# Kernel optimization log

Hardware: AMD Instinct MI355X
Metric: run time of the kernel (lower is better)

Reference implementation:

```python
import jax, jax.numpy as jnp
import numpy as np

E = 256
NH = 8
HD = E // NH
N, L, H, W = 8, 300, 96, 96


def setup_inputs() -> dict:
    key = jax.random.key(0)
    ks = jax.random.split(key, 9)
    s = 0.02
    return {
        "query_row": jax.random.normal(ks[0], (N, L, E), jnp.float32),
        "query_col": jax.random.normal(ks[1], (N, L, E), jnp.float32),
        "key_row": jax.random.normal(ks[2], (N, H, W, E), jnp.float32),
        "key_col": jax.random.normal(ks[3], (N, H, W, E), jnp.float32),
        "value": jax.random.normal(ks[4], (N, H, W, E), jnp.float32),
        "in_proj_weight": jax.random.normal(ks[5], (5 * E, E), jnp.float32) * s,
        "in_proj_bias": jax.random.normal(ks[6], (5 * E,), jnp.float32) * s,
        "out_proj_weight": jax.random.normal(ks[7], (E, E), jnp.float32) * s,
        "out_proj_bias": jax.random.normal(ks[8], (E,), jnp.float32) * s,
    }


def reference(query_row, query_col, key_row, key_col, value,
              in_proj_weight, in_proj_bias, out_proj_weight, out_proj_bias):
    n, l, e = query_row.shape
    _, h, w, _ = value.shape
    scale = float(HD) ** -0.5

    def proj(x, i):
        wi = in_proj_weight[i * E:(i + 1) * E]
        bi = in_proj_bias[i * E:(i + 1) * E]
        return x @ wi.T + bi

    q_row = proj(query_row, 0) * scale              # (N,L,E)
    q_col = proj(query_col, 1) * scale              # (N,L,E)
    k_row = proj(key_row, 2).mean(axis=1)           # (N,W,E)  mean over H
    k_col = proj(key_col, 3).mean(axis=2)           # (N,H,E)  mean over W
    v = proj(value, 4)                              # (N,H,W,E)

    qr = q_row.reshape(n, l, NH, HD)
    qc = q_col.reshape(n, l, NH, HD)
    kr = k_row.reshape(n, w, NH, HD)
    kc = k_col.reshape(n, h, NH, HD)
    vh = v.reshape(n, h, w, NH, HD)

    # row/col attention scores, softmax over source axis
    a_row = jax.nn.softmax(jnp.einsum('nled,nwed->nelw', qr, kr), axis=-1)  # (N,NH,L,W)
    a_col = jax.nn.softmax(jnp.einsum('nled,nhed->nelh', qc, kc), axis=-1)  # (N,NH,L,H)

    # col-then-row contraction (original else-branch: src_len_col >= src_len_row)
    out_col = jnp.einsum('nelh,nhwed->nelwd', a_col, vh)   # (N,NH,L,W,HD)
    out = jnp.einsum('nelw,nelwd->nled', a_row, out_col)    # (N,L,NH,HD)

    attn_output = out.transpose(1, 0, 2, 3).reshape(l, n, e)  # (L,N,E)
    return attn_output @ out_proj_weight.T + out_proj_bias
```

## Files before the change

### kernel.cpp

```cpp
#include <hip/hip_runtime.h>
#include <stdint.h>

typedef unsigned short u16;
typedef unsigned int   u32;
typedef __attribute__((ext_vector_type(8))) short bf16x8;
typedef __attribute__((ext_vector_type(4))) float f32x4;

static constexpr float kScale = 0.17677669529663687f;

__device__ __forceinline__ float bfl(u32 dw){ union{u32 u; float f;} x; x.u = dw << 16;        return x.f; }
__device__ __forceinline__ float bfh(u32 dw){ union{u32 u; float f;} x; x.u = dw & 0xffff0000u; return x.f; }
__device__ __forceinline__ float bf2f(u16 v){ union{u32 u; float f;} x; x.u = ((u32)v) << 16;  return x.f; }
__device__ __forceinline__ u16  f2bf(float f){
  union{float f; u32 u;} x; x.f = f;
  u32 r = x.u + 0x7fffu + ((x.u >> 16) & 1u);
  return (u16)(r >> 16);
}

__global__ void detect_kernel(const u16* __restrict__ bias, int* __restrict__ flag){
  int tid = threadIdx.x;
  u16 raw = bias[tid * 2];
  int big = (fabsf(bf2f(raw)) > 1e6f) ? 1 : 0;
  if ((raw & 0x7F80u) == 0x7F80u) big = 1;
  #pragma unroll
  for (int m = 1; m < 64; m <<= 1) big |= __shfl_xor(big, m);
  if (tid == 0) *flag = big;
}

__global__ __launch_bounds__(256) void prep_weights_kernel(
    const void* __restrict__ in_w, const void* __restrict__ out_w,
    u16* __restrict__ Wbf, const int* __restrict__ flag){
  const bool isf32 = (*flag != 0);
  int idx = blockIdx.x * 256 + threadIdx.x;
  size_t off = (size_t)idx * 8;
  const size_t IN_ELEMS = (size_t)1280 * 256;
  bool isout = off >= IN_ELEMS;
  const void* src = isout ? out_w : in_w;
  size_t soff = isout ? off - IN_ELEMS : off;
  u16 xl[8];
  if (isf32){
    const float* p = (const float*)src + soff;
    float4 f0 = *(const float4*)p;
    float4 f1 = *(const float4*)(p + 4);
    xl[0]=f2bf(f0.x); xl[1]=f2bf(f0.y); xl[2]=f2bf(f0.z); xl[3]=f2bf(f0.w);
    xl[4]=f2bf(f1.x); xl[5]=f2bf(f1.y); xl[6]=f2bf(f1.z); xl[7]=f2bf(f1.w);
  } else {
    *(uint4*)xl = *(const uint4*)((const u16*)src + soff);
  }
  *(uint4*)(Wbf + off) = *(uint4*)xl;
}

__global__ void means_kernel(const void* __restrict__ key_row, const void* __restrict__ key_col,
                             float* __restrict__ krm, float* __restrict__ kcm,
                             const int* __restrict__ flag){
  const bool isf32 = (*flag != 0);
  int g   = blockIdx.x * 256 + threadIdx.x;
  int c8  = (g & 31) * 8;
  int ri  = g >> 5;
  int rw  = ri % 96;
  int n   = ri / 96;
  float acc[8];
  #pragma unroll
  for (int i = 0; i < 8; i++) acc[i] = 0.f;

  size_t base, stride;
  const void* src;
  float* dst;
  if (blockIdx.y == 0){
    src    = key_row;
    base   = ((size_t)(n*96)*96 + rw)*256 + c8;
    stride = (size_t)96*256;
    dst    = krm + ((size_t)(n*96) + rw)*256 + c8;
  } else {
    src    = key_col;
    base   = ((size_t)(n*96) + rw)*(size_t)(96*256) + c8;
    stride = 256;
    dst    = kcm + ((size_t)(n*96) + rw)*256 + c8;
  }

  if (isf32){
    const float* p = (const float*)src + base;
    for (int t = 0; t < 96; t++){
      float4 f0 = *(const float4*)(p + t*stride);
      float4 f1 = *(const float4*)(p + t*stride + 4);
      acc[0]+=f0.x; acc[1]+=f0.y; acc[2]+=f0.z; acc[3]+=f0.w;
      acc[4]+=f1.x; acc[5]+=f1.y; acc[6]+=f1.z; acc[7]+=f1.w;
    }
  } else {
    const u16* p = (const u16*)src + base;
    for (int t = 0; t < 96; t++){
      uint4 u = *(const uint4*)(p + t*stride);
      acc[0]+=bfl(u.x); acc[1]+=bfh(u.x); acc[2]+=bfl(u.y); acc[3]+=bfh(u.y);
      acc[4]+=bfl(u.z); acc[5]+=bfh(u.z); acc[6]+=bfl(u.w); acc[7]+=bfh(u.w);
    }
  }
  #pragma unroll
  for (int i = 0; i < 8; i++) dst[i] = acc[i] * (1.f/96.f);
}

template<int XF, int OBF, int OMAP>
__global__ __launch_bounds__(256) void mfma_proj3(
    const void* __restrict__ Xv0, const void* __restrict__ Xv1,
    const u16* __restrict__ Wbf, int wr00, int wr01,
    const void* __restrict__ Bv, int bo0, int bo1,
    void* __restrict__ Yv0, void* __restrict__ Yv1,
    int M, float scale, int head0, int hg,
    const int* __restrict__ flag){
  const bool isf32 = (*flag != 0);
  const bool xf32  = (XF == 0) || (XF == 2 && isf32);
  __shared__ __align__(16) u16 Xs[64*40];
  __shared__ __align__(16) u16 Ws[64*40];
  __shared__ __align__(16) u16 stile[(OMAP==3) ? 64*66 : 64];

  const void* Xv  = blockIdx.z ? Xv1 : Xv0;
  const int wrow0 = blockIdx.z ? wr01 : wr00;
  const int boff  = blockIdx.z ? bo1  : bo0;
  void* Yv        = blockIdx.z ? Yv1 : Yv0;

  int tid = threadIdx.x;
  int m0  = blockIdx.x * 64;
  int j0  = blockIdx.y * 64;
  int wv  = tid >> 6;
  int ln  = tid & 63;
  int l15 = ln & 15;
  int quad = ln >> 4;
  int mh  = wv & 1;
  int nh  = wv >> 1;

  int srow = tid >> 2;
  int sko  = (tid & 3) * 8;

  f32x4 acc[2][2] = {{{0.f,0.f,0.f,0.f},{0.f,0.f,0.f,0.f}},
                     {{0.f,0.f,0.f,0.f},{0.f,0.f,0.f,0.f}}};

  int gm = m0 + srow;
  int wrel = j0 + srow;
  if (OMAP == 3){ wrel += head0*32; if (wrel > 255) wrel = 255; }
  const u16* wsrc = Wbf + (size_t)(wrow0 + wrel)*256 + sko;

  for (int p = 0; p < 8; p++){
    int k0 = p * 32;
    u16 xl[8];
    if (gm < M){
      size_t xoff = (size_t)gm*256 + k0 + sko;
      if (xf32){
        const float* xp = (const float*)Xv + xoff;
        float4 f0 = *(const float4*)xp;
        float4 f1 = *(const float4*)(xp + 4);
        xl[0]=f2bf(f0.x); xl[1]=f2bf(f0.y); xl[2]=f2bf(f0.z); xl[3]=f2bf(f0.w);
        xl[4]=f2bf(f1.x); xl[5]=f2bf(f1.y); xl[6]=f2bf(f1.z); xl[7]=f2bf(f1.w);
      } else {
        *(uint4*)xl = *(const uint4*)((const u16*)Xv + xoff);
      }
    } else {
      #pragma unroll
      for (int i = 0; i < 8; i++) xl[i] = 0;
    }
    uint4 wl = *(const uint4*)(wsrc + k0);
    __syncthreads();
    *(uint4*)(Xs + srow*40 + sko) = *(uint4*)xl;
    *(uint4*)(Ws + srow*40 + sko) = wl;
    __syncthreads();

    bf16x8 a0 = *(const bf16x8*)(Xs + (mh*32 +      l15)*40 + quad*8);
    bf16x8 a1 = *(const bf16x8*)(Xs + (mh*32 + 16 + l15)*40 + quad*8);
    bf16x8 b0 = *(const bf16x8*)(Ws + (nh*32 +      l15)*40 + quad*8);
    bf16x8 b1 = *(const bf16x8*)(Ws + (nh*32 + 16 + l15)*40 + quad*8);
    acc[0][0] = __builtin_amdgcn_mfma_f32_16x16x32_bf16(a0, b0, acc[0][0], 0,0,0);
    acc[0][1] = __builtin_amdgcn_mfma_f32_16x16x32_bf16(a0, b1, acc[0][1], 0,0,0);
    acc[1][0] = __builtin_amdgcn_mfma_f32_16x16x32_bf16(a1, b0, acc[1][0], 0,0,0);
    acc[1][1] = __builtin_amdgcn_mfma_f32_16x16x32_bf16(a1, b1, acc[1][1], 0,0,0);
  }

  float bv[2];
  #pragma unroll
  for (int tj = 0; tj < 2; tj++){
    int bidx = j0 + nh*32 + tj*16 + l15;
    if (OMAP == 3 && bidx > hg*32 - 1) bidx = hg*32 - 1;
    bv[tj] = isf32 ? ((const float*)Bv)[boff + bidx] : bf2f(((const u16*)Bv)[boff + bidx]);
  }

  if (OMAP == 3){
    __syncthreads();
    #pragma unroll
    for (int ti = 0; ti < 2; ti++)
      #pragma unroll
      for (int tj = 0; tj < 2; tj++)
        #pragma unroll
        for (int reg = 0; reg < 4; reg++)
          stile[(mh*32 + ti*16 + quad*4 + reg)*66 + nh*32 + tj*16 + l15] =
              f2bf(scale * (acc[ti][tj][reg] + bv[tj]));
    __syncthreads();
    int hw_i = tid & 63;
    int m    = m0 + hw_i;
    int nn   = m / 9216;
    int hwin = m - nn*9216;
    int hh   = hwin / 96, ww = hwin - hh*96;
    #pragma unroll
    for (int e = 0; e < 16; e++){
      int d_col = (tid >> 6) * 16 + e;
      int col   = j0 + d_col;
      if (col < hg*32){
        int gsv = nn*hg + (col >> 5), d = col & 31;
        ((u16*)Yv)[ (((size_t)gsv*96 + hh)*32 + d)*96 + ww ] = stile[hw_i*66 + d_col];
      }
    }
    return;
  }

  #pragma unroll
  for (int ti = 0; ti < 2; ti++)
    #pragma unroll
    for (int tj = 0; tj < 2; tj++)
      #pragma unroll
      for (int reg = 0; reg < 4; reg++){
        int m = m0 + mh*32 + ti*16 + quad*4 + reg;
        if (m >= M) continue;
        int col = j0 + nh*32 + tj*16 + l15;
        float vval = scale * (acc[ti][tj][reg] + bv[tj]);
        int orow = (OMAP == 1) ? ((m % 300)*8 + (m / 300)) : m;
        size_t oidx = (size_t)orow*256 + col;
        if (OBF == 2){
          if (isf32) ((float*)Yv)[oidx] = vval; else ((u16*)Yv)[oidx] = f2bf(vval);
        } else if (OBF == 1) ((u16*)Yv)[oidx] = f2bf(vval);
        else                 ((float*)Yv)[oidx] = vval;
      }
}

__global__ __launch_bounds__(64) void attn_weights_kernel(
    const u16* __restrict__ qr, const float* __restrict__ kr,
    const u16* __restrict__ qc, const float* __restrict__ kc,
    u16* __restrict__ arow, u16* __restrict__ acol,
    int head0, int hg){
  __shared__ float qs[30*32];
  int lt = blockIdx.x;
  int gs = blockIdx.y;
  int n  = gs / hg;
  int head = head0 + (gs % hg);
  const u16*   q = blockIdx.z ? qc : qr;
  const float* k = blockIdx.z ? kc : kr;
  u16*         a = blockIdx.z ? acol : arow;
  int lane = threadIdx.x;
  int l0   = lt * 30;

  for (int i = lane; i < 960; i += 64){
    int li = i >> 5, d = i & 31;
    qs[i] = bf2f(q[((size_t)(n*300) + l0 + li)*256 + head*32 + d]);
  }

  bool has2 = (lane < 32);
  float k1[32], k2[32];
  {
    const float* kp = k + ((size_t)(n*96) + lane)*256 + head*32;
    #pragma unroll
    for (int d4 = 0; d4 < 8; d4++){
      float4 f = *(const float4*)(kp + d4*4);
      k1[d4*4+0]=f.x; k1[d4*4+1]=f.y; k1[d4*4+2]=f.z; k1[d4*4+3]=f.w;
    }
    int w2c = has2 ? (64 + lane) : 95;
    const float* kp2 = k + ((size_t)(n*96) + w2c)*256 + head*32;
    #pragma unroll
    for (int d4 = 0; d4 < 8; d4++){
      float4 f = *(const float4*)(kp2 + d4*4);
      k2[d4*4+0]=f.x; k2[d4*4+1]=f.y; k2[d4*4+2]=f.z; k2[d4*4+3]=f.w;
    }
  }
  __syncthreads();

  for (int li = 0; li < 30; li++){
    const float* qv = qs + li*32;
    float s1 = 0.f, s2 = 0.f;
    #pragma unroll
    for (int d4 = 0; d4 < 8; d4++){
      float4 f = *(const float4*)(qv + d4*4);
      s1 += f.x*k1[d4*4+0] + f.y*k1[d4*4+1] + f.z*k1[d4*4+2] + f.w*k1[d4*4+3];
      s2 += f.x*k2[d4*4+0] + f.y*k2[d4*4+1] + f.z*k2[d4*4+2] + f.w*k2[d4*4+3];
    }
    float m = fmaxf(s1, has2 ? s2 : -1e30f);
    #pragma unroll
    for (int mask = 1; mask < 64; mask <<= 1) m = fmaxf(m, __shfl_xor(m, mask));
    float e1 = __expf(s1 - m);
    float e2 = has2 ? __expf(s2 - m) : 0.f;
    float s  = e1 + e2;
    #pragma unroll
    for (int mask = 1; mask < 64; mask <<= 1) s += __shfl_xor(s, mask);
    float inv = 1.f / s;
    u16* dst = a + ((size_t)gs*300 + l0 + li)*96;
    dst[lane] = f2bf(e1 * inv);
    if (has2) dst[64 + lane] = f2bf(e2 * inv);
  }
}

__global__ __launch_bounds__(256) void rcda_core_kernel(
    const u16* __restrict__ arow, const u16* __restrict__ acol,
    const u16* __restrict__ v, u16* __restrict__ attn, int head0, int hg){
  __shared__ __align__(16) u16 vt[4*32*104];
  __shared__ __align__(16) u16 aw[32*96];
  __shared__ float cs[32*97];
  __shared__ float red[2*64*8];

  int b   = blockIdx.x;
  int xcd = b & 7;
  int jj  = b >> 3;
  int lt  = jj % 10;
  int gg  = jj / 10;
  int gs  = gg*8 + xcd;
  int n   = gs / hg;
  int head = head0 + (gs % hg);
  int l0  = lt * 32;
  int tid = threadIdx.x;
  int wv  = tid >> 6;
  int ln  = tid & 63;
  int l15 = ln & 15;
  int quad = ln >> 4;
  int nt  = wv & 1;
  int hp  = wv >> 1;

  for (int i = tid; i < 384; i += 256){
    int row = i / 12, rem = i - row*12;
    int lc = l0 + row; if (lc > 299) lc = 299;
    *(uint4*)(aw + row*96 + rem*8) = *(const uint4*)(arow + ((size_t)gs*300 + lc)*96 + rem*8);
  }
  for (int i = tid; i < 3072; i += 256){
    int row = i / 96, col = i - row*96;
    int lc = l0 + row; if (lc > 299) lc = 299;
    cs[row*97 + col] = bf2f(acol[((size_t)gs*300 + lc)*96 + col]);
  }
  __syncthreads();

  bf16x8 afr[2][3];
  #pragma unroll
  for (int mt = 0; mt < 2; mt++)
    #pragma unroll
    for (int ks = 0; ks < 3; ks++)
      afr[mt][ks] = *(const bf16x8*)(aw + (mt*16 + l15)*96 + ks*32 + quad*8);

  f32x4 out[2] = {{0.f,0.f,0.f,0.f},{0.f,0.f,0.f,0.f}};
  const u16* vbase = v + (size_t)gs * 96*32*96;

  for (int cc = 0; cc < 24; cc++){
    __syncthreads();
    const uint4* gsrc = (const uint4*)(vbase + (size_t)cc * 4*32*96);
    #pragma unroll
    for (int it = 0; it < 6; it++){
      int i = tid + it*256;
      int row = i / 12, rem = i - row*12;
      *(uint4*)((char*)vt + row*208 + rem*16) = gsrc[i];
    }
    __syncthreads();

    #pragma unroll
    for (int hh = 0; hh < 2; hh++){
      int h = hp*2 + hh;
      bf16x8 bfr[3];
      #pragma unroll
      for (int ks = 0; ks < 3; ks++)
        bfr[ks] = *(const bf16x8*)(vt + (h*32 + nt*16 + l15)*104 + ks*32 + quad*8);
      int habs = cc*4 + h;
      #pragma unroll
      for (int mt = 0; mt < 2; mt++){
        f32x4 t = {0.f,0.f,0.f,0.f};
        t = __builtin_amdgcn_mfma_f32_16x16x32_bf16(afr[mt][0], bfr[0], t, 0,0,0);
        t = __builtin_amdgcn_mfma_f32_16x16x32_bf16(afr[mt][1], bfr[1], t, 0,0,0);
        t = __builtin_amdgcn_mfma_f32_16x16x32_bf16(afr[mt][2], bfr[2], t, 0,0,0);
        #pragma unroll
        for (int reg = 0; reg < 4; reg++){
          float sc = cs[(mt*16 + quad*4 + reg)*97 + habs];
          out[mt][reg] += sc * t[reg];
        }
      }
    }
  }

  __syncthreads();
  if (hp == 1){
    float* r = red + ((size_t)(nt*64 + ln))*8;
    #pragma unroll
    for (int mt = 0; mt < 2; mt++)
      #pragma unroll
      for (int reg = 0; reg < 4; reg++) r[mt*4 + reg] = out[mt][reg];
  }
  __syncthreads();
  if (hp == 0){
    const float* r = red + ((size_t)(nt*64 + ln))*8;
    #pragma unroll
    for (int mt = 0; mt < 2; mt++){
      #pragma unroll
      for (int reg = 0; reg < 4; reg++){
        int l = l0 + mt*16 + quad*4 + reg;
        if (l < 300)
          attn[((size_t)(n*300) + l)*256 + head*32 + nt*16 + l15] =
              f2bf(out[mt][reg] + r[mt*4 + reg]);
      }
    }
  }
}

extern "C" void kernel_launch(void* const* d_in, const int* in_sizes, int n_in,
                              void* d_out, int out_size, void* d_ws, size_t ws_size,
                              hipStream_t stream){
  const void* query_row = d_in[0];
  const void* query_col = d_in[1];
  const void* key_row   = d_in[2];
  const void* key_col   = d_in[3];
  const void* value     = d_in[4];
  const void* in_w      = d_in[5];
  const void* in_b      = d_in[6];
  const void* out_w     = d_in[7];
  const void* out_b     = d_in[8];

  int hg = 1;
  {
    const size_t fixed = 7618816, per = 5640192;
    if      (ws_size >= fixed + 8*per) hg = 8;
    else if (ws_size >= fixed + 4*per) hg = 4;
    else if (ws_size >= fixed + 2*per) hg = 2;
    else                               hg = 1;
  }

  char* ws = (char*)d_ws;
  int*  flag = (int*)ws;
  size_t SV = (size_t)hg * 8 * 9216 * 32 * 2;
  size_t SA = (size_t)hg * 8 * 300 * 96 * 2;
  size_t off = 256;
  u16*   v_slab = (u16*)(ws + off); off += SV;
  u16*   arow   = (u16*)(ws + off); off += SA;
  u16*   acol   = (u16*)(ws + off); off += SA;
  u16*   Wbf    = (u16*)(ws + off); off += 786432;
  u16*   qr     = (u16*)(ws + off); off += 1228800;
  u16*   qc     = (u16*)(ws + off); off += 1228800;
  float* krm    = (float*)(ws + off); off += 786432;
  float* kcm    = (float*)(ws + off); off += 786432;
  float* kr     = (float*)(ws + off); off += 786432;
  float* kc     = (float*)(ws + off); off += 786432;
  u16*   attnb  = (u16*)(ws + off); off += 1228800;

  detect_kernel<<<1, 64, 0, stream>>>((const u16*)in_b, flag);

  prep_weights_kernel<<<192, 256, 0, stream>>>(in_w, out_w, Wbf, flag);

  means_kernel<<<dim3(96, 2), 256, 0, stream>>>(key_row, key_col, krm, kcm, flag);

  mfma_proj3<2,1,0><<<dim3(38, 4, 2), 256, 0, stream>>>(
      query_row, query_col, Wbf, 0, 256, in_b, 0, 256, qr, qc,
      2400, kScale, 0, hg, flag);

  mfma_proj3<0,0,0><<<dim3(12, 4, 2), 256, 0, stream>>>(
      krm, kcm, Wbf, 512, 768, in_b, 512, 768, kr, kc,
      768, 1.f, 0, hg, flag);

  for (int head0 = 0; head0 < 8; head0 += hg){
    int gy = (hg*32 + 63) / 64;
    mfma_proj3<2,1,3><<<dim3(1152, gy, 1), 256, 0, stream>>>(
        value, value, Wbf, 1024, 1024, in_b, 1024 + head0*32, 1024 + head0*32,
        v_slab, v_slab, 73728, 1.f, head0, hg, flag);
    attn_weights_kernel<<<dim3(10, 8*hg, 2), 64, 0, stream>>>(qr, kr, qc, kc, arow, acol, head0, hg);
    rcda_core_kernel<<<dim3(10 * 8 * hg), 256, 0, stream>>>(arow, acol, v_slab, attnb, head0, hg);
  }

  mfma_proj3<1,2,1><<<dim3(38, 4, 1), 256, 0, stream>>>(
      attnb, attnb, Wbf, 1280, 1280, out_b, 0, 0, d_out, d_out,
      2400, 1.f, 0, hg, flag);
}
```

Before: 365.2 us.

## Double-buffer LDS tiles in projection GEMM and widen means kernel parallelism

```diff
diff --git a/kernel.cpp b/kernel.cpp
--- a/kernel.cpp
+++ b/kernel.cpp
@@ -50,56 +50,55 @@
   *(uint4*)(Wbf + off) = *(uint4*)xl;
 }
 
-__global__ void means_kernel(const void* __restrict__ key_row, const void* __restrict__ key_col,
-                             float* __restrict__ krm, float* __restrict__ kcm,
-                             const int* __restrict__ flag){
+__global__ __launch_bounds__(256) void means_kernel(
+    const void* __restrict__ key_row, const void* __restrict__ key_col,
+    float* __restrict__ krm, float* __restrict__ kcm,
+    const int* __restrict__ flag){
   const bool isf32 = (*flag != 0);
-  int g   = blockIdx.x * 256 + threadIdx.x;
-  int c8  = (g & 31) * 8;
-  int ri  = g >> 5;
-  int rw  = ri % 96;
-  int n   = ri / 96;
-  float acc[8];
-  #pragma unroll
-  for (int i = 0; i < 8; i++) acc[i] = 0.f;
+  int tid = threadIdx.x;
+  int r2  = tid >> 7;
+  int cc  = (tid & 127) * 2;
+  int row = blockIdx.x * 2 + r2;
+  int n   = row / 96;
+  int rw  = row - n*96;
 
   size_t base, stride;
   const void* src;
   float* dst;
   if (blockIdx.y == 0){
     src    = key_row;
-    base   = ((size_t)(n*96)*96 + rw)*256 + c8;
+    base   = ((size_t)(n*96)*96 + rw)*256 + cc;
     stride = (size_t)96*256;
-    dst    = krm + ((size_t)(n*96) + rw)*256 + c8;
+    dst    = krm + (size_t)row*256 + cc;
   } else {
     src    = key_col;
-    base   = ((size_t)(n*96) + rw)*(size_t)(96*256) + c8;
+    base   = ((size_t)(n*96) + rw)*(size_t)(96*256) + cc;
     stride = 256;
-    dst    = kcm + ((size_t)(n*96) + rw)*256 + c8;
-  }
-
+    dst    = kcm + (size_t)row*256 + cc;
+  }
+
+  float a0 = 0.f, a1 = 0.f;
   if (isf32){
     const float* p = (const float*)src + base;
+    #pragma unroll 4
     for (int t = 0; t < 96; t++){
-      float4 f0 = *(const float4*)(p + t*stride);
-      float4 f1 = *(const float4*)(p + t*stride + 4);
-      acc[0]+=f0.x; acc[1]+=f0.y; acc[2]+=f0.z; acc[3]+=f0.w;
-      acc[4]+=f1.x; acc[5]+=f1.y; acc[6]+=f1.z; acc[7]+=f1.w;
+      float2 f = *(const float2*)(p + t*stride);
+      a0 += f.x; a1 += f.y;
     }
   } else {
     const u16* p = (const u16*)src + base;
+    #pragma unroll 4
     for (int t = 0; t < 96; t++){
-      uint4 u = *(const uint4*)(p + t*stride);
-      acc[0]+=bfl(u.x); acc[1]+=bfh(u.x); acc[2]+=bfl(u.y); acc[3]+=bfh(u.y);
-      acc[4]+=bfl(u.z); acc[5]+=bfh(u.z); acc[6]+=bfl(u.w); acc[7]+=bfh(u.w);
-    }
-  }
-  #pragma unroll
-  for (int i = 0; i < 8; i++) dst[i] = acc[i] * (1.f/96.f);
+      u32 u = *(const u32*)(p + t*stride);
+      a0 += bfl(u); a1 += bfh(u);
+    }
+  }
+  dst[0] = a0 * (1.f/96.f);
+  dst[1] = a1 * (1.f/96.f);
 }
 
 template<int XF, int OBF, int OMAP>
-__global__ __launch_bounds__(256) void mfma_proj3(
+__global__ __launch_bounds__(256) void mfma_proj4(
     const void* __restrict__ Xv0, const void* __restrict__ Xv1,
     const u16* __restrict__ Wbf, int wr00, int wr01,
     const void* __restrict__ Bv, int bo0, int bo1,
@@ -108,8 +107,8 @@
     const int* __restrict__ flag){
   const bool isf32 = (*flag != 0);
   const bool xf32  = (XF == 0) || (XF == 2 && isf32);
-  __shared__ __align__(16) u16 Xs[64*40];
-  __shared__ __align__(16) u16 Ws[64*40];
+  __shared__ __align__(16) u16 Xs[2][64*40];
+  __shared__ __align__(16) u16 Ws[2][64*40];
   __shared__ __align__(16) u16 stile[(OMAP==3) ? 64*66 : 64];
 
   const void* Xv  = blockIdx.z ? Xv1 : Xv0;
@@ -133,43 +132,78 @@
   f32x4 acc[2][2] = {{{0.f,0.f,0.f,0.f},{0.f,0.f,0.f,0.f}},
                      {{0.f,0.f,0.f,0.f},{0.f,0.f,0.f,0.f}}};
 
-  int gm = m0 + srow;
+  const int gm = m0 + srow;
   int wrel = j0 + srow;
   if (OMAP == 3){ wrel += head0*32; if (wrel > 255) wrel = 255; }
   const u16* wsrc = Wbf + (size_t)(wrow0 + wrel)*256 + sko;
-
-  for (int p = 0; p < 8; p++){
-    int k0 = p * 32;
+  const bool xok  = (gm < M);
+  const size_t xrow = (size_t)gm*256 + sko;
+
+  {
     u16 xl[8];
-    if (gm < M){
-      size_t xoff = (size_t)gm*256 + k0 + sko;
+    if (xok){
       if (xf32){
-        const float* xp = (const float*)Xv + xoff;
+        const float* xp = (const float*)Xv + xrow;
         float4 f0 = *(const float4*)xp;
         float4 f1 = *(const float4*)(xp + 4);
         xl[0]=f2bf(f0.x); xl[1]=f2bf(f0.y); xl[2]=f2bf(f0.z); xl[3]=f2bf(f0.w);
         xl[4]=f2bf(f1.x); xl[5]=f2bf(f1.y); xl[6]=f2bf(f1.z); xl[7]=f2bf(f1.w);
       } else {
-        *(uint4*)xl = *(const uint4*)((const u16*)Xv + xoff);
+        *(uint4*)xl = *(const uint4*)((const u16*)Xv + xrow);
       }
     } else {
       #pragma unroll
       for (int i = 0; i < 8; i++) xl[i] = 0;
     }
-    uint4 wl = *(const uint4*)(wsrc + k0);
+    *(uint4*)(Xs[0] + srow*40 + sko) = *(uint4*)xl;
+    *(uint4*)(Ws[0] + srow*40 + sko) = *(const uint4*)(wsrc);
+  }
+
+  #pragma unroll
+  for (int p = 0; p < 8; p++){
+    const int cur = p & 1, nxt = cur ^ 1;
     __syncthreads();
-    *(uint4*)(Xs + srow*40 + sko) = *(uint4*)xl;
-    *(uint4*)(Ws + srow*40 + sko) = wl;
-    __syncthreads();
-
-    bf16x8 a0 = *(const bf16x8*)(Xs + (mh*32 +      l15)*40 + quad*8);
-    bf16x8 a1 = *(const bf16x8*)(Xs + (mh*32 + 16 + l15)*40 + quad*8);
-    bf16x8 b0 = *(const bf16x8*)(Ws + (nh*32 +      l15)*40 + quad*8);
-    bf16x8 b1 = *(const bf16x8*)(Ws + (nh*32 + 16 + l15)*40 + quad*8);
+
+    float4 f0n, f1n; uint4 xun; uint4 wln;
+    if (p < 7){
+      const int k1 = (p+1)*32;
+      if (xok){
+        if (xf32){
+          const float* xp = (const float*)Xv + xrow + k1;
+          f0n = *(const float4*)xp;
+          f1n = *(const float4*)(xp + 4);
+        } else {
+          xun = *(const uint4*)((const u16*)Xv + xrow + k1);
+        }
+      }
+      wln = *(const uint4*)(wsrc + k1);
+    }
+
+    bf16x8 a0 = *(const bf16x8*)(Xs[cur] + (mh*32 +      l15)*40 + quad*8);
+    bf16x8 a1 = *(const bf16x8*)(Xs[cur] + (mh*32 + 16 + l15)*40 + quad*8);
+    bf16x8 b0 = *(const bf16x8*)(Ws[cur] + (nh*32 +      l15)*40 + quad*8);
+    bf16x8 b1 = *(const bf16x8*)(Ws[cur] + (nh*32 + 16 + l15)*40 + quad*8);
     acc[0][0] = __builtin_amdgcn_mfma_f32_16x16x32_bf16(a0, b0, acc[0][0], 0,0,0);
     acc[0][1] = __builtin_amdgcn_mfma_f32_16x16x32_bf16(a0, b1, acc[0][1], 0,0,0);
     acc[1][0] = __builtin_amdgcn_mfma_f32_16x16x32_bf16(a1, b0, acc[1][0], 0,0,0);
     acc[1][1] = __builtin_amdgcn_mfma_f32_16x16x32_bf16(a1, b1, acc[1][1], 0,0,0);
+
+    if (p < 7){
+      u16 xl[8];
+      if (xok){
+        if (xf32){
+          xl[0]=f2bf(f0n.x); xl[1]=f2bf(f0n.y); xl[2]=f2bf(f0n.z); xl[3]=f2bf(f0n.w);
+          xl[4]=f2bf(f1n.x); xl[5]=f2bf(f1n.y); xl[6]=f2bf(f1n.z); xl[7]=f2bf(f1n.w);
+        } else {
+          *(uint4*)xl = xun;
+        }
+      } else {
+        #pragma unroll
+        for (int i = 0; i < 8; i++) xl[i] = 0;
+      }
+      *(uint4*)(Xs[nxt] + srow*40 + sko) = *(uint4*)xl;
+      *(uint4*)(Ws[nxt] + srow*40 + sko) = wln;
+    }
   }
 
   float bv[2];
@@ -439,26 +473,26 @@
 
   prep_weights_kernel<<<192, 256, 0, stream>>>(in_w, out_w, Wbf, flag);
 
-  means_kernel<<<dim3(96, 2), 256, 0, stream>>>(key_row, key_col, krm, kcm, flag);
-
-  mfma_proj3<2,1,0><<<dim3(38, 4, 2), 256, 0, stream>>>(
+  means_kernel<<<dim3(384, 2), 256, 0, stream>>>(key_row, key_col, krm, kcm, flag);
+
+  mfma_proj4<2,1,0><<<dim3(38, 4, 2), 256, 0, stream>>>(
       query_row, query_col, Wbf, 0, 256, in_b, 0, 256, qr, qc,
       2400, kScale, 0, hg, flag);
 
-  mfma_proj3<0,0,0><<<dim3(12, 4, 2), 256, 0, stream>>>(
+  mfma_proj4<0,0,0><<<dim3(12, 4, 2), 256, 0, stream>>>(
       krm, kcm, Wbf, 512, 768, in_b, 512, 768, kr, kc,
       768, 1.f, 0, hg, flag);
 
   for (int head0 = 0; head0 < 8; head0 += hg){
     int gy = (hg*32 + 63) / 64;
-    mfma_proj3<2,1,3><<<dim3(1152, gy, 1), 256, 0, stream>>>(
+    mfma_proj4<2,1,3><<<dim3(1152, gy, 1), 256, 0, stream>>>(
         value, value, Wbf, 1024, 1024, in_b, 1024 + head0*32, 1024 + head0*32,
         v_slab, v_slab, 73728, 1.f, head0, hg, flag);
     attn_weights_kernel<<<dim3(10, 8*hg, 2), 64, 0, stream>>>(qr, kr, qc, kc, arow, acol, head0, hg);
     rcda_core_kernel<<<dim3(10 * 8 * hg), 256, 0, stream>>>(arow, acol, v_slab, attnb, head0, hg);
   }
 
-  mfma_proj3<1,2,1><<<dim3(38, 4, 1), 256, 0, stream>>>(
+  mfma_proj4<1,2,1><<<dim3(38, 4, 1), 256, 0, stream>>>(
       attnb, attnb, Wbf, 1280, 1280, out_b, 0, 0, d_out, d_out,
       2400, 1.f, 0, hg, flag);
 }
```

Measured after the change: 372.0 us. No clear change (+1.9%).

## Add specialized value projection kernel covering all heads per block; widen means grid

Applied to the files above, without the earlier changes.

```diff
diff --git a/kernel.cpp b/kernel.cpp
--- a/kernel.cpp
+++ b/kernel.cpp
@@ -50,52 +50,51 @@
   *(uint4*)(Wbf + off) = *(uint4*)xl;
 }
 
-__global__ void means_kernel(const void* __restrict__ key_row, const void* __restrict__ key_col,
-                             float* __restrict__ krm, float* __restrict__ kcm,
-                             const int* __restrict__ flag){
+__global__ __launch_bounds__(256) void means_kernel(
+    const void* __restrict__ key_row, const void* __restrict__ key_col,
+    float* __restrict__ krm, float* __restrict__ kcm,
+    const int* __restrict__ flag){
   const bool isf32 = (*flag != 0);
-  int g   = blockIdx.x * 256 + threadIdx.x;
-  int c8  = (g & 31) * 8;
-  int ri  = g >> 5;
-  int rw  = ri % 96;
-  int n   = ri / 96;
-  float acc[8];
-  #pragma unroll
-  for (int i = 0; i < 8; i++) acc[i] = 0.f;
+  int tid = threadIdx.x;
+  int r2  = tid >> 7;
+  int cc  = (tid & 127) * 2;
+  int row = blockIdx.x * 2 + r2;
+  int n   = row / 96;
+  int rw  = row - n*96;
 
   size_t base, stride;
   const void* src;
   float* dst;
   if (blockIdx.y == 0){
     src    = key_row;
-    base   = ((size_t)(n*96)*96 + rw)*256 + c8;
+    base   = ((size_t)(n*96)*96 + rw)*256 + cc;
     stride = (size_t)96*256;
-    dst    = krm + ((size_t)(n*96) + rw)*256 + c8;
+    dst    = krm + (size_t)row*256 + cc;
   } else {
     src    = key_col;
-    base   = ((size_t)(n*96) + rw)*(size_t)(96*256) + c8;
+    base   = ((size_t)(n*96) + rw)*(size_t)(96*256) + cc;
     stride = 256;
-    dst    = kcm + ((size_t)(n*96) + rw)*256 + c8;
-  }
-
+    dst    = kcm + (size_t)row*256 + cc;
+  }
+
+  float a0 = 0.f, a1 = 0.f;
   if (isf32){
     const float* p = (const float*)src + base;
+    #pragma unroll 4
     for (int t = 0; t < 96; t++){
-      float4 f0 = *(const float4*)(p + t*stride);
-      float4 f1 = *(const float4*)(p + t*stride + 4);
-      acc[0]+=f0.x; acc[1]+=f0.y; acc[2]+=f0.z; acc[3]+=f0.w;
-      acc[4]+=f1.x; acc[5]+=f1.y; acc[6]+=f1.z; acc[7]+=f1.w;
+      float2 f = *(const float2*)(p + t*stride);
+      a0 += f.x; a1 += f.y;
     }
   } else {
     const u16* p = (const u16*)src + base;
+    #pragma unroll 4
     for (int t = 0; t < 96; t++){
-      uint4 u = *(const uint4*)(p + t*stride);
-      acc[0]+=bfl(u.x); acc[1]+=bfh(u.x); acc[2]+=bfl(u.y); acc[3]+=bfh(u.y);
-      acc[4]+=bfl(u.z); acc[5]+=bfh(u.z); acc[6]+=bfl(u.w); acc[7]+=bfh(u.w);
-    }
-  }
-  #pragma unroll
-  for (int i = 0; i < 8; i++) dst[i] = acc[i] * (1.f/96.f);
+      u32 u = *(const u32*)(p + t*stride);
+      a0 += bfl(u); a1 += bfh(u);
+    }
+  }
+  dst[0] = a0 * (1.f/96.f);
+  dst[1] = a1 * (1.f/96.f);
 }
 
 template<int XF, int OBF, int OMAP>
@@ -225,6 +224,113 @@
         } else if (OBF == 1) ((u16*)Yv)[oidx] = f2bf(vval);
         else                 ((float*)Yv)[oidx] = vval;
       }
+}
+
+template<int NJ>
+__global__ __launch_bounds__(256) void vproj_kernel(
+    const void* __restrict__ Xv, const u16* __restrict__ Wbf, int wbase,
+    const void* __restrict__ Bv, int boff, u16* __restrict__ Yv,
+    int hg, const int* __restrict__ flag){
+  const bool xf32 = (*flag != 0);
+  constexpr int WS_ELE = (NJ*64*40 > 64*66) ? NJ*64*40 : 64*66;
+  __shared__ __align__(16) u16 Xs[64*40];
+  __shared__ __align__(16) u16 Ws[WS_ELE];
+  u16* stile = Ws;
+
+  int tid = threadIdx.x;
+  int m0  = blockIdx.x * 64;
+  int wv  = tid >> 6;
+  int ln  = tid & 63;
+  int l15 = ln & 15;
+  int quad = ln >> 4;
+  int mh  = wv & 1;
+  int nh  = wv >> 1;
+
+  int srow = tid >> 2;
+  int sko  = (tid & 3) * 8;
+
+  f32x4 acc[NJ][2][2];
+  #pragma unroll
+  for (int jt = 0; jt < NJ; jt++)
+    #pragma unroll
+    for (int i = 0; i < 2; i++)
+      #pragma unroll
+      for (int j = 0; j < 2; j++)
+        acc[jt][i][j] = (f32x4){0.f,0.f,0.f,0.f};
+
+  const int gm = m0 + srow;
+  const size_t xrow = (size_t)gm*256 + sko;
+  const u16* wsrc = Wbf + (size_t)(wbase + srow)*256 + sko;
+
+  for (int p = 0; p < 8; p++){
+    const int k0 = p * 32;
+    u16 xl[8];
+    if (xf32){
+      const float* xp = (const float*)Xv + xrow + k0;
+      float4 f0 = *(const float4*)xp;
+      float4 f1 = *(const float4*)(xp + 4);
+      xl[0]=f2bf(f0.x); xl[1]=f2bf(f0.y); xl[2]=f2bf(f0.z); xl[3]=f2bf(f0.w);
+      xl[4]=f2bf(f1.x); xl[5]=f2bf(f1.y); xl[6]=f2bf(f1.z); xl[7]=f2bf(f1.w);
+    } else {
+      *(uint4*)xl = *(const uint4*)((const u16*)Xv + xrow + k0);
+    }
+    uint4 wl[NJ];
+    #pragma unroll
+    for (int it = 0; it < NJ; it++)
+      wl[it] = *(const uint4*)(wsrc + (size_t)it*64*256 + k0);
+    __syncthreads();
+    *(uint4*)(Xs + srow*40 + sko) = *(uint4*)xl;
+    #pragma unroll
+    for (int it = 0; it < NJ; it++)
+      *(uint4*)(Ws + (it*64 + srow)*40 + sko) = wl[it];
+    __syncthreads();
+
+    bf16x8 a0 = *(const bf16x8*)(Xs + (mh*32 +      l15)*40 + quad*8);
+    bf16x8 a1 = *(const bf16x8*)(Xs + (mh*32 + 16 + l15)*40 + quad*8);
+    #pragma unroll
+    for (int jt = 0; jt < NJ; jt++){
+      bf16x8 b0 = *(const bf16x8*)(Ws + (jt*64 + nh*32 +      l15)*40 + quad*8);
+      bf16x8 b1 = *(const bf16x8*)(Ws + (jt*64 + nh*32 + 16 + l15)*40 + quad*8);
+      acc[jt][0][0] = __builtin_amdgcn_mfma_f32_16x16x32_bf16(a0, b0, acc[jt][0][0], 0,0,0);
+      acc[jt][0][1] = __builtin_amdgcn_mfma_f32_16x16x32_bf16(a0, b1, acc[jt][0][1], 0,0,0);
+      acc[jt][1][0] = __builtin_amdgcn_mfma_f32_16x16x32_bf16(a1, b0, acc[jt][1][0], 0,0,0);
+      acc[jt][1][1] = __builtin_amdgcn_mfma_f32_16x16x32_bf16(a1, b1, acc[jt][1][1], 0,0,0);
+    }
+  }
+
+  const bool isf32 = xf32;
+  int hw_i = ln;
+  int m    = m0 + hw_i;
+  int nn   = m / 9216;
+  int hwin = m - nn*9216;
+  int hh   = hwin / 96, ww = hwin - hh*96;
+
+  #pragma unroll
+  for (int jt = 0; jt < NJ; jt++){
+    float bv[2];
+    #pragma unroll
+    for (int tj = 0; tj < 2; tj++){
+      int col = jt*64 + nh*32 + tj*16 + l15;
+      bv[tj] = isf32 ? ((const float*)Bv)[boff + col] : bf2f(((const u16*)Bv)[boff + col]);
+    }
+    __syncthreads();
+    #pragma unroll
+    for (int ti = 0; ti < 2; ti++)
+      #pragma unroll
+      for (int tj = 0; tj < 2; tj++)
+        #pragma unroll
+        for (int reg = 0; reg < 4; reg++)
+          stile[(mh*32 + ti*16 + quad*4 + reg)*66 + nh*32 + tj*16 + l15] =
+              f2bf(acc[jt][ti][tj][reg] + bv[tj]);
+    __syncthreads();
+    #pragma unroll
+    for (int e = 0; e < 16; e++){
+      int d_col = wv*16 + e;
+      int col   = jt*64 + d_col;
+      int gsv = nn*hg + (col >> 5), d = col & 31;
+      Yv[ (((size_t)gsv*96 + hh)*32 + d)*96 + ww ] = stile[hw_i*66 + d_col];
+    }
+  }
 }
 
 __global__ __launch_bounds__(64) void attn_weights_kernel(
@@ -439,7 +545,7 @@
 
   prep_weights_kernel<<<192, 256, 0, stream>>>(in_w, out_w, Wbf, flag);
 
-  means_kernel<<<dim3(96, 2), 256, 0, stream>>>(key_row, key_col, krm, kcm, flag);
+  means_kernel<<<dim3(384, 2), 256, 0, stream>>>(key_row, key_col, krm, kcm, flag);
 
   mfma_proj3<2,1,0><<<dim3(38, 4, 2), 256, 0, stream>>>(
       query_row, query_col, Wbf, 0, 256, in_b, 0, 256, qr, qc,
@@ -450,10 +556,17 @@
       768, 1.f, 0, hg, flag);
 
   for (int head0 = 0; head0 < 8; head0 += hg){
-    int gy = (hg*32 + 63) / 64;
-    mfma_proj3<2,1,3><<<dim3(1152, gy, 1), 256, 0, stream>>>(
-        value, value, Wbf, 1024, 1024, in_b, 1024 + head0*32, 1024 + head0*32,
-        v_slab, v_slab, 73728, 1.f, head0, hg, flag);
+    int wb = 1024 + head0*32;
+    if (hg == 8)
+      vproj_kernel<4><<<1152, 256, 0, stream>>>(value, Wbf, wb, in_b, wb, v_slab, hg, flag);
+    else if (hg == 4)
+      vproj_kernel<2><<<1152, 256, 0, stream>>>(value, Wbf, wb, in_b, wb, v_slab, hg, flag);
+    else if (hg == 2)
+      vproj_kernel<1><<<1152, 256, 0, stream>>>(value, Wbf, wb, in_b, wb, v_slab, hg, flag);
+    else
+      mfma_proj3<2,1,3><<<dim3(1152, 1, 1), 256, 0, stream>>>(
+          value, value, Wbf, 1024, 1024, in_b, wb, wb,
+          v_slab, v_slab, 73728, 1.f, head0, hg, flag);
     attn_weights_kernel<<<dim3(10, 8*hg, 2), 64, 0, stream>>>(qr, kr, qc, kc, arow, acol, head0, hg);
     rcda_core_kernel<<<dim3(10 * 8 * hg), 256, 0, stream>>>(arow, acol, v_slab, attnb, head0, hg);
   }
```

Result: slower. 391.4 us (+7.2%).

## Fuse weight prep with key means and merge all input projections into one launch

Applied to the files above, without the earlier changes.

```diff
diff --git a/kernel.cpp b/kernel.cpp
--- a/kernel.cpp
+++ b/kernel.cpp
@@ -27,99 +27,89 @@
   if (tid == 0) *flag = big;
 }
 
-__global__ __launch_bounds__(256) void prep_weights_kernel(
+__global__ __launch_bounds__(256) void prep_means_kernel(
     const void* __restrict__ in_w, const void* __restrict__ out_w,
-    u16* __restrict__ Wbf, const int* __restrict__ flag){
+    u16* __restrict__ Wbf,
+    const void* __restrict__ key_row, const void* __restrict__ key_col,
+    float* __restrict__ krm, float* __restrict__ kcm,
+    const int* __restrict__ flag){
   const bool isf32 = (*flag != 0);
-  int idx = blockIdx.x * 256 + threadIdx.x;
-  size_t off = (size_t)idx * 8;
-  const size_t IN_ELEMS = (size_t)1280 * 256;
-  bool isout = off >= IN_ELEMS;
-  const void* src = isout ? out_w : in_w;
-  size_t soff = isout ? off - IN_ELEMS : off;
-  u16 xl[8];
-  if (isf32){
-    const float* p = (const float*)src + soff;
-    float4 f0 = *(const float4*)p;
-    float4 f1 = *(const float4*)(p + 4);
-    xl[0]=f2bf(f0.x); xl[1]=f2bf(f0.y); xl[2]=f2bf(f0.z); xl[3]=f2bf(f0.w);
-    xl[4]=f2bf(f1.x); xl[5]=f2bf(f1.y); xl[6]=f2bf(f1.z); xl[7]=f2bf(f1.w);
-  } else {
-    *(uint4*)xl = *(const uint4*)((const u16*)src + soff);
-  }
-  *(uint4*)(Wbf + off) = *(uint4*)xl;
-}
-
-__global__ void means_kernel(const void* __restrict__ key_row, const void* __restrict__ key_col,
-                             float* __restrict__ krm, float* __restrict__ kcm,
-                             const int* __restrict__ flag){
-  const bool isf32 = (*flag != 0);
-  int g   = blockIdx.x * 256 + threadIdx.x;
-  int c8  = (g & 31) * 8;
-  int ri  = g >> 5;
-  int rw  = ri % 96;
-  int n   = ri / 96;
-  float acc[8];
-  #pragma unroll
-  for (int i = 0; i < 8; i++) acc[i] = 0.f;
+  int bx = blockIdx.x;
+  int tid = threadIdx.x;
+
+  if (bx < 192){
+    int idx = bx * 256 + tid;
+    size_t off = (size_t)idx * 8;
+    const size_t IN_ELEMS = (size_t)1280 * 256;
+    bool isout = off >= IN_ELEMS;
+    const void* src = isout ? out_w : in_w;
+    size_t soff = isout ? off - IN_ELEMS : off;
+    u16 xl[8];
+    if (isf32){
+      const float* p = (const float*)src + soff;
+      float4 f0 = *(const float4*)p;
+      float4 f1 = *(const float4*)(p + 4);
+      xl[0]=f2bf(f0.x); xl[1]=f2bf(f0.y); xl[2]=f2bf(f0.z); xl[3]=f2bf(f0.w);
+      xl[4]=f2bf(f1.x); xl[5]=f2bf(f1.y); xl[6]=f2bf(f1.z); xl[7]=f2bf(f1.w);
+    } else {
+      *(uint4*)xl = *(const uint4*)((const u16*)src + soff);
+    }
+    *(uint4*)(Wbf + off) = *(uint4*)xl;
+    return;
+  }
+
+  int bm  = bx - 192;
+  int mb  = bm % 384;
+  int sel = bm / 384;
+  int r2  = tid >> 7;
+  int cc  = (tid & 127) * 2;
+  int row = mb * 2 + r2;
+  int n   = row / 96;
+  int rw  = row - n*96;
 
   size_t base, stride;
   const void* src;
   float* dst;
-  if (blockIdx.y == 0){
+  if (sel == 0){
     src    = key_row;
-    base   = ((size_t)(n*96)*96 + rw)*256 + c8;
+    base   = ((size_t)(n*96)*96 + rw)*256 + cc;
     stride = (size_t)96*256;
-    dst    = krm + ((size_t)(n*96) + rw)*256 + c8;
+    dst    = krm + (size_t)row*256 + cc;
   } else {
     src    = key_col;
-    base   = ((size_t)(n*96) + rw)*(size_t)(96*256) + c8;
+    base   = ((size_t)(n*96) + rw)*(size_t)(96*256) + cc;
     stride = 256;
-    dst    = kcm + ((size_t)(n*96) + rw)*256 + c8;
-  }
-
+    dst    = kcm + (size_t)row*256 + cc;
+  }
+
+  float a0 = 0.f, a1 = 0.f;
   if (isf32){
     const float* p = (const float*)src + base;
+    #pragma unroll 4
     for (int t = 0; t < 96; t++){
-      float4 f0 = *(const float4*)(p + t*stride);
-      float4 f1 = *(const float4*)(p + t*stride + 4);
-      acc[0]+=f0.x; acc[1]+=f0.y; acc[2]+=f0.z; acc[3]+=f0.w;
-      acc[4]+=f1.x; acc[5]+=f1.y; acc[6]+=f1.z; acc[7]+=f1.w;
+      float2 f = *(const float2*)(p + t*stride);
+      a0 += f.x; a1 += f.y;
     }
   } else {
     const u16* p = (const u16*)src + base;
+    #pragma unroll 4
     for (int t = 0; t < 96; t++){
-      uint4 u = *(const uint4*)(p + t*stride);
-      acc[0]+=bfl(u.x); acc[1]+=bfh(u.x); acc[2]+=bfl(u.y); acc[3]+=bfh(u.y);
-      acc[4]+=bfl(u.z); acc[5]+=bfh(u.z); acc[6]+=bfl(u.w); acc[7]+=bfh(u.w);
-    }
-  }
-  #pragma unroll
-  for (int i = 0; i < 8; i++) dst[i] = acc[i] * (1.f/96.f);
-}
-
-template<int XF, int OBF, int OMAP>
-__global__ __launch_bounds__(256) void mfma_proj3(
-    const void* __restrict__ Xv0, const void* __restrict__ Xv1,
-    const u16* __restrict__ Wbf, int wr00, int wr01,
-    const void* __restrict__ Bv, int bo0, int bo1,
-    void* __restrict__ Yv0, void* __restrict__ Yv1,
-    int M, float scale, int head0, int hg,
-    const int* __restrict__ flag){
-  const bool isf32 = (*flag != 0);
-  const bool xf32  = (XF == 0) || (XF == 2 && isf32);
-  __shared__ __align__(16) u16 Xs[64*40];
-  __shared__ __align__(16) u16 Ws[64*40];
-  __shared__ __align__(16) u16 stile[(OMAP==3) ? 64*66 : 64];
-
-  const void* Xv  = blockIdx.z ? Xv1 : Xv0;
-  const int wrow0 = blockIdx.z ? wr01 : wr00;
-  const int boff  = blockIdx.z ? bo1  : bo0;
-  void* Yv        = blockIdx.z ? Yv1 : Yv0;
-
+      u32 u = *(const u32*)(p + t*stride);
+      a0 += bfl(u); a1 += bfh(u);
+    }
+  }
+  dst[0] = a0 * (1.f/96.f);
+  dst[1] = a1 * (1.f/96.f);
+}
+
+__device__ __forceinline__ void proj_core(
+    const void* __restrict__ Xv, bool xf32,
+    const u16* __restrict__ Wbf, int wrow0, int wrel_add,
+    const void* __restrict__ Bv, bool bvf32, int boff,
+    void* __restrict__ Yv, int obf, int omap,
+    int m0, int j0, int M, float scale, int hg,
+    u16* __restrict__ Xs, u16* __restrict__ Ws, u16* __restrict__ stile){
   int tid = threadIdx.x;
-  int m0  = blockIdx.x * 64;
-  int j0  = blockIdx.y * 64;
   int wv  = tid >> 6;
   int ln  = tid & 63;
   int l15 = ln & 15;
@@ -135,7 +125,7 @@
 
   int gm = m0 + srow;
   int wrel = j0 + srow;
-  if (OMAP == 3){ wrel += head0*32; if (wrel > 255) wrel = 255; }
+  if (omap == 3){ wrel += wrel_add; if (wrel > 255) wrel = 255; }
   const u16* wsrc = Wbf + (size_t)(wrow0 + wrel)*256 + sko;
 
   for (int p = 0; p < 8; p++){
@@ -176,11 +166,11 @@
   #pragma unroll
   for (int tj = 0; tj < 2; tj++){
     int bidx = j0 + nh*32 + tj*16 + l15;
-    if (OMAP == 3 && bidx > hg*32 - 1) bidx = hg*32 - 1;
-    bv[tj] = isf32 ? ((const float*)Bv)[boff + bidx] : bf2f(((const u16*)Bv)[boff + bidx]);
-  }
-
-  if (OMAP == 3){
+    if (omap == 3 && bidx > hg*32 - 1) bidx = hg*32 - 1;
+    bv[tj] = bvf32 ? ((const float*)Bv)[boff + bidx] : bf2f(((const u16*)Bv)[boff + bidx]);
+  }
+
+  if (omap == 3){
     __syncthreads();
     #pragma unroll
     for (int ti = 0; ti < 2; ti++)
@@ -218,13 +208,74 @@
         if (m >= M) continue;
         int col = j0 + nh*32 + tj*16 + l15;
         float vval = scale * (acc[ti][tj][reg] + bv[tj]);
-        int orow = (OMAP == 1) ? ((m % 300)*8 + (m / 300)) : m;
+        int orow = (omap == 1) ? ((m % 300)*8 + (m / 300)) : m;
         size_t oidx = (size_t)orow*256 + col;
-        if (OBF == 2){
-          if (isf32) ((float*)Yv)[oidx] = vval; else ((u16*)Yv)[oidx] = f2bf(vval);
-        } else if (OBF == 1) ((u16*)Yv)[oidx] = f2bf(vval);
-        else                 ((float*)Yv)[oidx] = vval;
+        if (obf == 1) ((u16*)Yv)[oidx] = f2bf(vval);
+        else          ((float*)Yv)[oidx] = vval;
       }
+}
+
+template<int XF, int OBF, int OMAP>
+__global__ __launch_bounds__(256) void mfma_proj3(
+    const void* __restrict__ Xv0, const void* __restrict__ Xv1,
+    const u16* __restrict__ Wbf, int wr00, int wr01,
+    const void* __restrict__ Bv, int bo0, int bo1,
+    void* __restrict__ Yv0, void* __restrict__ Yv1,
+    int M, float scale, int head0, int hg,
+    const int* __restrict__ flag){
+  __shared__ __align__(16) u16 Xs[64*40];
+  __shared__ __align__(16) u16 Ws[64*40];
+  __shared__ __align__(16) u16 stile[(OMAP==3) ? 64*66 : 64];
+  const bool isf32 = (*flag != 0);
+  const bool xf32  = (XF == 0) || (XF == 2 && isf32);
+  const int  obf   = (OBF == 2) ? (isf32 ? 0 : 1) : OBF;
+  proj_core(blockIdx.z ? Xv1 : Xv0, xf32,
+            Wbf, blockIdx.z ? wr01 : wr00, head0*32,
+            Bv, isf32, blockIdx.z ? bo1 : bo0,
+            blockIdx.z ? Yv1 : Yv0, obf, OMAP,
+            blockIdx.x*64, blockIdx.y*64, M, scale, hg,
+            Xs, Ws, stile);
+}
+
+__global__ __launch_bounds__(256, 8) void mega_proj_kernel(
+    const void* __restrict__ query_row, const void* __restrict__ query_col,
+    const float* __restrict__ krm, const float* __restrict__ kcm,
+    const void* __restrict__ value,
+    const u16* __restrict__ Wbf, const void* __restrict__ in_b,
+    u16* __restrict__ qr, u16* __restrict__ qc,
+    float* __restrict__ kr, float* __restrict__ kc,
+    u16* __restrict__ v_slab,
+    const int* __restrict__ flag){
+  __shared__ __align__(16) u16 Xs[64*40];
+  __shared__ __align__(16) u16 Ws[64*40];
+  __shared__ __align__(16) u16 stile[64*66];
+  const bool isf32 = (*flag != 0);
+  const int bx = blockIdx.x;
+
+  if (bx < 4608){
+    int m0 = (bx % 1152) * 64;
+    int j0 = (bx / 1152) * 64;
+    proj_core(value, isf32, Wbf, 1024, 0, in_b, isf32, 1024,
+              v_slab, 1, 3, m0, j0, 73728, 1.f, 8, Xs, Ws, stile);
+  } else if (bx < 4912){
+    int bq = bx - 4608;
+    int qx = bq % 38;
+    int qy = (bq / 38) & 3;
+    int qz = bq / 152;
+    proj_core(qz ? query_col : query_row, isf32,
+              Wbf, qz ? 256 : 0, 0, in_b, isf32, qz ? 256 : 0,
+              qz ? (void*)qc : (void*)qr, 1, 0,
+              qx*64, qy*64, 2400, kScale, 8, Xs, Ws, stile);
+  } else {
+    int bk = bx - 4912;
+    int kx = bk % 12;
+    int ky = (bk / 12) & 3;
+    int kz = bk / 48;
+    proj_core(kz ? (const void*)kcm : (const void*)krm, true,
+              Wbf, kz ? 768 : 512, 0, in_b, isf32, kz ? 768 : 512,
+              kz ? (void*)kc : (void*)kr, 0, 0,
+              kx*64, ky*64, 768, 1.f, 8, Xs, Ws, stile);
+  }
 }
 
 __global__ __launch_bounds__(64) void attn_weights_kernel(
@@ -437,25 +488,31 @@
 
   detect_kernel<<<1, 64, 0, stream>>>((const u16*)in_b, flag);
 
-  prep_weights_kernel<<<192, 256, 0, stream>>>(in_w, out_w, Wbf, flag);
-
-  means_kernel<<<dim3(96, 2), 256, 0, stream>>>(key_row, key_col, krm, kcm, flag);
-
-  mfma_proj3<2,1,0><<<dim3(38, 4, 2), 256, 0, stream>>>(
-      query_row, query_col, Wbf, 0, 256, in_b, 0, 256, qr, qc,
-      2400, kScale, 0, hg, flag);
-
-  mfma_proj3<0,0,0><<<dim3(12, 4, 2), 256, 0, stream>>>(
-      krm, kcm, Wbf, 512, 768, in_b, 512, 768, kr, kc,
-      768, 1.f, 0, hg, flag);
-
-  for (int head0 = 0; head0 < 8; head0 += hg){
-    int gy = (hg*32 + 63) / 64;
-    mfma_proj3<2,1,3><<<dim3(1152, gy, 1), 256, 0, stream>>>(
-        value, value, Wbf, 1024, 1024, in_b, 1024 + head0*32, 1024 + head0*32,
-        v_slab, v_slab, 73728, 1.f, head0, hg, flag);
-    attn_weights_kernel<<<dim3(10, 8*hg, 2), 64, 0, stream>>>(qr, kr, qc, kc, arow, acol, head0, hg);
-    rcda_core_kernel<<<dim3(10 * 8 * hg), 256, 0, stream>>>(arow, acol, v_slab, attnb, head0, hg);
+  prep_means_kernel<<<960, 256, 0, stream>>>(in_w, out_w, Wbf,
+                                             key_row, key_col, krm, kcm, flag);
+
+  if (hg == 8){
+    mega_proj_kernel<<<5008, 256, 0, stream>>>(
+        query_row, query_col, krm, kcm, value, Wbf, in_b,
+        qr, qc, kr, kc, v_slab, flag);
+    attn_weights_kernel<<<dim3(10, 64, 2), 64, 0, stream>>>(qr, kr, qc, kc, arow, acol, 0, 8);
+    rcda_core_kernel<<<dim3(640), 256, 0, stream>>>(arow, acol, v_slab, attnb, 0, 8);
+  } else {
+    mfma_proj3<2,1,0><<<dim3(38, 4, 2), 256, 0, stream>>>(
+        query_row, query_col, Wbf, 0, 256, in_b, 0, 256, qr, qc,
+        2400, kScale, 0, hg, flag);
+    mfma_proj3<0,0,0><<<dim3(12, 4, 2), 256, 0, stream>>>(
+        krm, kcm, Wbf, 512, 768, in_b, 512, 768, kr, kc,
+        768, 1.f, 0, hg, flag);
+    for (int head0 = 0; head0 < 8; head0 += hg){
+      int gy = (hg*32 + 63) / 64;
+      int wb = 1024 + head0*32;
+      mfma_proj3<2,1,3><<<dim3(1152, gy, 1), 256, 0, stream>>>(
+          value, value, Wbf, 1024, 1024, in_b, wb, wb,
+          v_slab, v_slab, 73728, 1.f, head0, hg, flag);
+      attn_weights_kernel<<<dim3(10, 8*hg, 2), 64, 0, stream>>>(qr, kr, qc, kc, arow, acol, head0, hg);
+      rcda_core_kernel<<<dim3(10 * 8 * hg), 256, 0, stream>>>(arow, acol, v_slab, attnb, head0, hg);
+    }
   }
 
   mfma_proj3<1,2,1><<<dim3(38, 4, 1), 256, 0, stream>>>(
```

Result: faster. 344.9 us (-5.6%).
